# Kernel tuning notes

Hardware: AMD Instinct MI355X
Metric: run time of the kernel (lower is better)

The kernel has to match this reference:

```python
import jax, jax.numpy as jnp
import numpy as np

N_NODES = 100000
N_EDGES = 3200000
D_IN = 128
D_OUT = 128
EPS = 0.0  # GINConv default eps, not trained


def setup_inputs() -> dict:
    key = jax.random.key(0)
    k1, k2, k3, k4, k5, k6, k7 = jax.random.split(key, 7)
    x = jax.random.normal(k1, (N_NODES, D_IN), dtype=jnp.float32)
    edge_index = jax.random.randint(k2, (2, N_EDGES), 0, N_NODES, dtype=jnp.int64)
    # MLP params: Linear(D_IN->D_OUT), ReLU, Linear(D_OUT->D_OUT)
    s1 = 1.0 / np.sqrt(D_IN)
    s2 = 1.0 / np.sqrt(D_OUT)
    W1 = jax.random.uniform(k3, (D_IN, D_OUT), jnp.float32, -s1, s1)
    b1 = jax.random.uniform(k4, (D_OUT,), jnp.float32, -s1, s1)
    W2 = jax.random.uniform(k5, (D_OUT, D_OUT), jnp.float32, -s2, s2)
    b2 = jax.random.uniform(k6, (D_OUT,), jnp.float32, -s2, s2)
    return {"x": x, "edge_index": edge_index, "W1": W1, "b1": b1, "W2": W2, "b2": b2}


def reference(x, edge_index, W1, b1, W2, b2):
    src, dst = edge_index[0], edge_index[1]
    # message = x[src]; aggregate by sum onto dst (source_to_target flow)
    agg = jax.ops.segment_sum(x[src], dst, num_segments=x.shape[0])  # [N, D_IN]
    h = (1.0 + EPS) * x + agg
    h = jax.nn.relu(h @ W1 + b1)
    return h @ W2 + b2
```

## Files before the change

### kernel.cpp

```cpp
#include <hip/hip_runtime.h>

#define D 128
#define TILE_ROWS 64
#define MLP_THREADS 512
#define SCAN_THREADS 1024
#define BK_NODES 128
#define MAX_BKT 1024
#define EPB 16
#define SC_THREADS 512
#define SC_EPB 24
#define CAPL 6144
#define FMLP_THREADS 512
#define MLP_BM 128
#define HSTR 136

typedef unsigned short ushort_t;
typedef unsigned int uint_t;
typedef __attribute__((ext_vector_type(8))) short short8v;
typedef __attribute__((ext_vector_type(4))) float f32x4;

__device__ __forceinline__ ushort_t f2bf(float f) {
    uint_t u = __float_as_uint(f);
    u = u + 0x7FFFu + ((u >> 16) & 1u);
    return (ushort_t)(u >> 16);
}
__device__ __forceinline__ float bf_lo(uint_t u) { return __uint_as_float(u << 16); }
__device__ __forceinline__ float bf_hi(uint_t u) { return __uint_as_float(u & 0xffff0000u); }

__global__ void cast_kernel(const float* __restrict__ x, ushort_t* __restrict__ xh, int n4) {
    int i = blockIdx.x * blockDim.x + threadIdx.x;
    if (i < n4) {
        float4 v = reinterpret_cast<const float4*>(x)[i];
        ushort4 o;
        o.x = f2bf(v.x); o.y = f2bf(v.y); o.z = f2bf(v.z); o.w = f2bf(v.w);
        reinterpret_cast<ushort4*>(xh)[i] = o;
    }
}

__global__ void wprep_kernel(const float* __restrict__ W1, const float* __restrict__ W2,
                             ushort_t* __restrict__ w1t, ushort_t* __restrict__ w2t) {
    int i = blockIdx.x * blockDim.x + threadIdx.x;
    if (i < D * D) {
        int c = i & 127, k = i >> 7;
        w1t[(size_t)c * HSTR + k] = f2bf(W1[(size_t)k * D + c]);
        w2t[(size_t)c * HSTR + k] = f2bf(W2[(size_t)k * D + c]);
    }
}

__global__ void zero_kernel(int* __restrict__ p, int n) {
    int i = blockIdx.x * blockDim.x + threadIdx.x;
    if (i < n) p[i] = 0;
}

__global__ void coarse_hist_kernel(const int* __restrict__ dsts,
                                   int* __restrict__ ghist, int ne, int nbkt) {
    __shared__ int h[MAX_BKT];
    for (int k = threadIdx.x; k < nbkt; k += blockDim.x) h[k] = 0;
    __syncthreads();
    int base = blockIdx.x * blockDim.x * EPB;
    for (int j = 0; j < EPB; ++j) {
        int e = base + j * blockDim.x + threadIdx.x;
        if (e < ne) atomicAdd(&h[dsts[e] >> 7], 1);
    }
    __syncthreads();
    for (int k = threadIdx.x; k < nbkt; k += blockDim.x)
        if (h[k]) atomicAdd(&ghist[k], h[k]);
}

__global__ __launch_bounds__(SCAN_THREADS) void coarse_scan_kernel(
    const int* __restrict__ ghist, int* __restrict__ cbase,
    int* __restrict__ ccursor, int* __restrict__ offsets,
    int nbkt, int nnodes, int ne) {
    __shared__ int sc[SCAN_THREADS];
    int t = threadIdx.x;
    int v = (t < nbkt) ? ghist[t] : 0;
    sc[t] = v;
    __syncthreads();
    for (int off = 1; off < SCAN_THREADS; off <<= 1) {
        int u = (t >= off) ? sc[t - off] : 0;
        __syncthreads();
        sc[t] += u;
        __syncthreads();
    }
    if (t < nbkt) { cbase[t] = sc[t] - v; ccursor[t] = sc[t] - v; }
    if (t == 0) { cbase[nbkt] = sc[SCAN_THREADS - 1]; offsets[nnodes] = ne; }
}

__global__ __launch_bounds__(SC_THREADS) void coarse_scatter_kernel(
    const int* __restrict__ ei, int* __restrict__ ccursor,
    int* __restrict__ pairs, int ne, int nbkt) {
    __shared__ int h[MAX_BKT];
    __shared__ int lbase[MAX_BKT];
    __shared__ int gbase[MAX_BKT];
    __shared__ int lcur[MAX_BKT];
    __shared__ int stot[SC_THREADS];
    __shared__ int stage[SC_THREADS * SC_EPB];

    const int t = threadIdx.x;
    const int base = blockIdx.x * SC_THREADS * SC_EPB;

    for (int k = t; k < MAX_BKT; k += SC_THREADS) h[k] = 0;
    __syncthreads();

    for (int j = 0; j < SC_EPB; ++j) {
        int e = base + j * SC_THREADS + t;
        if (e < ne) atomicAdd(&h[ei[ne + e] >> 7], 1);
    }
    __syncthreads();

    int a0 = h[2 * t], a1 = h[2 * t + 1];
    stot[t] = a0 + a1;
    __syncthreads();
    for (int off = 1; off < SC_THREADS; off <<= 1) {
        int u = (t >= off) ? stot[t - off] : 0;
        __syncthreads();
        stot[t] += u;
        __syncthreads();
    }
    int bexc = stot[t] - (a0 + a1);
    lbase[2 * t] = bexc;
    lbase[2 * t + 1] = bexc + a0;
    lcur[2 * t] = bexc;
    lcur[2 * t + 1] = bexc + a0;
    __syncthreads();

    for (int k = t; k < MAX_BKT; k += SC_THREADS)
        gbase[k] = h[k] ? atomicAdd(&ccursor[k], h[k]) : 0;
    __syncthreads();

    for (int j = 0; j < SC_EPB; ++j) {
        int e = base + j * SC_THREADS + t;
        if (e < ne) {
            int dst = ei[ne + e];
            int src = ei[e];
            int k = dst >> 7;
            int pos = atomicAdd(&lcur[k], 1);
            stage[pos] = (src << 7) | (dst & (BK_NODES - 1));
        }
    }
    __syncthreads();

    const int lane = t & 63, w = t >> 6;
    for (int k = w; k < nbkt; k += (SC_THREADS / 64)) {
        int cnt = h[k];
        int lb = lbase[k], gb = gbase[k];
        for (int i = lane; i < cnt; i += 64)
            pairs[gb + i] = stage[lb + i];
    }
}

__global__ void bucket_csr_kernel(const int* __restrict__ pairs,
                                  const int* __restrict__ cbase,
                                  int* __restrict__ offsets,
                                  int* __restrict__ sorted_src,
                                  int nnodes) {
    __shared__ int h[BK_NODES];
    __shared__ int ex[BK_NODES];
    __shared__ int cur[BK_NODES];
    __shared__ int stage[CAPL];
    int b = blockIdx.x;
    int t = threadIdx.x;
    int rbeg = cbase[b], rend = cbase[b + 1];
    int cnt = rend - rbeg;
    if (t < BK_NODES) h[t] = 0;
    __syncthreads();
    for (int i = rbeg + t; i < rend; i += blockDim.x)
        atomicAdd(&h[pairs[i] & (BK_NODES - 1)], 1);
    __syncthreads();
    if (t < BK_NODES) ex[t] = h[t];
    __syncthreads();
    for (int off = 1; off < BK_NODES; off <<= 1) {
        int u = (t >= off && t < BK_NODES) ? ex[t - off] : 0;
        __syncthreads();
        if (t < BK_NODES) ex[t] += u;
        __syncthreads();
    }
    const bool staged = (cnt <= CAPL);
    if (t < BK_NODES) {
        int e = ex[t] - h[t];
        cur[t] = staged ? e : rbeg + e;
        int node = b * BK_NODES + t;
        if (node < nnodes) offsets[node] = rbeg + e;
    }
    __syncthreads();
    if (staged) {
        for (int i = rbeg + t; i < rend; i += blockDim.x) {
            int p = pairs[i];
            int pos = atomicAdd(&cur[p & (BK_NODES - 1)], 1);
            stage[pos] = p >> 7;
        }
        __syncthreads();
        for (int i = t; i < cnt; i += blockDim.x)
            sorted_src[rbeg + i] = stage[i];
    } else {
        for (int i = rbeg + t; i < rend; i += blockDim.x) {
            int p = pairs[i];
            int pos = atomicAdd(&cur[p & (BK_NODES - 1)], 1);
            sorted_src[pos] = p >> 7;
        }
    }
}

__global__ void agg_bf_kernel(const ushort_t* __restrict__ xh,
                              const int* __restrict__ sorted_src,
                              const int* __restrict__ offsets,
                              float* __restrict__ out,
                              uint_t* __restrict__ hbf, int nnodes) {
    int gid = blockIdx.x * blockDim.x + threadIdx.x;
    int node = gid >> 6;
    if (node >= nnodes) return;
    const int lane = threadIdx.x & 63;
    const int col = lane & 31;
    const int half = lane >> 5;
    const uint2* xp = reinterpret_cast<const uint2*>(xh);
    int beg = offsets[node];
    int end = offsets[node + 1];

    float s0, s1, s2, s3;
    {
        uint2 u = xp[(size_t)node * 32 + col];
        if (half) { u.x = 0u; u.y = 0u; }
        s0 = bf_lo(u.x); s1 = bf_hi(u.x);
        s2 = bf_lo(u.y); s3 = bf_hi(u.y);
    }

    int i = beg;
    for (; i + 16 <= end; i += 16) {
        uint2 v0 = xp[(size_t)sorted_src[i + 0 + half] * 32 + col];
        uint2 v1 = xp[(size_t)sorted_src[i + 2 + half] * 32 + col];
        uint2 v2 = xp[(size_t)sorted_src[i + 4 + half] * 32 + col];
        uint2 v3 = xp[(size_t)sorted_src[i + 6 + half] * 32 + col];
        uint2 v4 = xp[(size_t)sorted_src[i + 8 + half] * 32 + col];
        uint2 v5 = xp[(size_t)sorted_src[i + 10 + half] * 32 + col];
        uint2 v6 = xp[(size_t)sorted_src[i + 12 + half] * 32 + col];
        uint2 v7 = xp[(size_t)sorted_src[i + 14 + half] * 32 + col];
        s0 += bf_lo(v0.x) + bf_lo(v1.x) + bf_lo(v2.x) + bf_lo(v3.x) +
              bf_lo(v4.x) + bf_lo(v5.x) + bf_lo(v6.x) + bf_lo(v7.x);
        s1 += bf_hi(v0.x) + bf_hi(v1.x) + bf_hi(v2.x) + bf_hi(v3.x) +
              bf_hi(v4.x) + bf_hi(v5.x) + bf_hi(v6.x) + bf_hi(v7.x);
        s2 += bf_lo(v0.y) + bf_lo(v1.y) + bf_lo(v2.y) + bf_lo(v3.y) +
              bf_lo(v4.y) + bf_lo(v5.y) + bf_lo(v6.y) + bf_lo(v7.y);
        s3 += bf_hi(v0.y) + bf_hi(v1.y) + bf_hi(v2.y) + bf_hi(v3.y) +
              bf_hi(v4.y) + bf_hi(v5.y) + bf_hi(v6.y) + bf_hi(v7.y);
    }
    for (; i + 2 <= end; i += 2) {
        uint2 u = xp[(size_t)sorted_src[i + half] * 32 + col];
        s0 += bf_lo(u.x); s1 += bf_hi(u.x);
        s2 += bf_lo(u.y); s3 += bf_hi(u.y);
    }
    if (i < end && half == 0) {
        uint2 u = xp[(size_t)sorted_src[i] * 32 + col];
        s0 += bf_lo(u.x); s1 += bf_hi(u.x);
        s2 += bf_lo(u.y); s3 += bf_hi(u.y);
    }

    s0 += __shfl_xor(s0, 32);
    s1 += __shfl_xor(s1, 32);
    s2 += __shfl_xor(s2, 32);
    s3 += __shfl_xor(s3, 32);

    if (half == 0) {
        if (hbf) {
            uint_t lo = (uint_t)f2bf(s0) | ((uint_t)f2bf(s1) << 16);
            uint_t hi = (uint_t)f2bf(s2) | ((uint_t)f2bf(s3) << 16);
            uint2 o; o.x = lo; o.y = hi;
            reinterpret_cast<uint2*>(hbf)[(size_t)node * 32 + col] = o;
        } else {
            float4 o; o.x = s0; o.y = s1; o.z = s2; o.w = s3;
            reinterpret_cast<float4*>(out + (size_t)node * D)[col] = o;
        }
    }
}

__global__ void agg_fp_kernel(const float* __restrict__ x,
                              const int* __restrict__ sorted_src,
                              const int* __restrict__ offsets,
                              float* __restrict__ out, int nnodes) {
    int gid = blockIdx.x * blockDim.x + threadIdx.x;
    int node = gid >> 6;
    if (node >= nnodes) return;
    int lane = threadIdx.x & 63;
    int beg = offsets[node];
    int end = offsets[node + 1];
    const float2* xp = reinterpret_cast<const float2*>(x);
    float2 a = xp[(size_t)node * 64 + lane];
    float sx = a.x, sy = a.y;
    int i = beg;
    for (; i + 8 <= end; i += 8) {
        int s0 = sorted_src[i + 0], s1 = sorted_src[i + 1];
        int s2 = sorted_src[i + 2], s3 = sorted_src[i + 3];
        int s4 = sorted_src[i + 4], s5 = sorted_src[i + 5];
        int s6 = sorted_src[i + 6], s7 = sorted_src[i + 7];
        float2 v0 = xp[(size_t)s0 * 64 + lane];
        float2 v1 = xp[(size_t)s1 * 64 + lane];
        float2 v2 = xp[(size_t)s2 * 64 + lane];
        float2 v3 = xp[(size_t)s3 * 64 + lane];
        float2 v4 = xp[(size_t)s4 * 64 + lane];
        float2 v5 = xp[(size_t)s5 * 64 + lane];
        float2 v6 = xp[(size_t)s6 * 64 + lane];
        float2 v7 = xp[(size_t)s7 * 64 + lane];
        sx += ((v0.x + v1.x) + (v2.x + v3.x)) + ((v4.x + v5.x) + (v6.x + v7.x));
        sy += ((v0.y + v1.y) + (v2.y + v3.y)) + ((v4.y + v5.y) + (v6.y + v7.y));
    }
    for (; i < end; ++i) {
        float2 v = xp[(size_t)sorted_src[i] * 64 + lane];
        sx += v.x;
        sy += v.y;
    }
    float2 o; o.x = sx; o.y = sy;
    reinterpret_cast<float2*>(out)[(size_t)node * 64 + lane] = o;
}

template <bool BF>
__global__ __launch_bounds__(FMLP_THREADS, 1) void fused_mlp_kernel(
    const float* __restrict__ h, const uint_t* __restrict__ hbf,
    const ushort_t* __restrict__ w1t, const ushort_t* __restrict__ w2t,
    const float* __restrict__ b1, const float* __restrict__ b2,
    float* __restrict__ outp, int nrows) {
    __shared__ ushort_t sh[MLP_BM * HSTR];
    __shared__ ushort_t sw1[D * HSTR];
    __shared__ ushort_t sw2[D * HSTR];
    const int tid = threadIdx.x;
    const int row0 = blockIdx.x * MLP_BM;

    {
        const uint4* s1 = reinterpret_cast<const uint4*>(w1t);
        const uint4* s2 = reinterpret_cast<const uint4*>(w2t);
        uint4* d1 = reinterpret_cast<uint4*>(sw1);
        uint4* d2 = reinterpret_cast<uint4*>(sw2);
        for (int i = tid; i < D * HSTR / 8; i += FMLP_THREADS) { d1[i] = s1[i]; d2[i] = s2[i]; }
    }
    if (BF) {
        for (int i = tid; i < MLP_BM * 16; i += FMLP_THREADS) {
            int r = i >> 4, c = i & 15;
            uint4 v = make_uint4(0u, 0u, 0u, 0u);
            if (row0 + r < nrows)
                v = reinterpret_cast<const uint4*>(hbf + (size_t)(row0 + r) * 64)[c];
            *reinterpret_cast<uint4*>(&sh[r * HSTR + c * 8]) = v;
        }
    } else {
        for (int i = tid; i < MLP_BM * 32; i += FMLP_THREADS) {
            int r = i >> 5, c4 = i & 31;
            float4 v = make_float4(0.f, 0.f, 0.f, 0.f);
            if (row0 + r < nrows)
                v = reinterpret_cast<const float4*>(h + (size_t)(row0 + r) * D)[c4];
            ushort4 o;
            o.x = f2bf(v.x); o.y = f2bf(v.y); o.z = f2bf(v.z); o.w = f2bf(v.w);
            *reinterpret_cast<ushort4*>(&sh[r * HSTR + c4 * 4]) = o;
        }
    }
    __syncthreads();

    const int w = tid >> 6, l = tid & 63;
    const int lr = l & 15, lg = l >> 4;
    const int rowb = w * 16;

    short8v A[4];
#pragma unroll
    for (int kk = 0; kk < 4; ++kk)
        A[kk] = *reinterpret_cast<const short8v*>(&sh[(rowb + lr) * HSTR + kk * 32 + lg * 8]);
#pragma unroll
    for (int n = 0; n < 8; ++n) {
        float bv = b1[n * 16 + lr];
        f32x4 acc = {bv, bv, bv, bv};
#pragma unroll
        for (int kk = 0; kk < 4; ++kk) {
            short8v B = *reinterpret_cast<const short8v*>(&sw1[(n * 16 + lr) * HSTR + kk * 32 + lg * 8]);
            acc = __builtin_amdgcn_mfma_f32_16x16x32_bf16(A[kk], B, acc, 0, 0, 0);
        }
#pragma unroll
        for (int r = 0; r < 4; ++r) {
            float v = fmaxf(acc[r], 0.f);
            sh[(rowb + lg * 4 + r) * HSTR + n * 16 + lr] = f2bf(v);
        }
    }

    short8v A2[4];
#pragma unroll
    for (int kk = 0; kk < 4; ++kk)
        A2[kk] = *reinterpret_cast<const short8v*>(&sh[(rowb + lr) * HSTR + kk * 32 + lg * 8]);
#pragma unroll
    for (int n = 0; n < 8; ++n) {
        float bv = b2[n * 16 + lr];
        f32x4 acc = {bv, bv, bv, bv};
#pragma unroll
        for (int kk = 0; kk < 4; ++kk) {
            short8v B = *reinterpret_cast<const short8v*>(&sw2[(n * 16 + lr) * HSTR + kk * 32 + lg * 8]);
            acc = __builtin_amdgcn_mfma_f32_16x16x32_bf16(A2[kk], B, acc, 0, 0, 0);
        }
#pragma unroll
        for (int r = 0; r < 4; ++r) {
            int grow = row0 + rowb + lg * 4 + r;
            if (grow < nrows)
                outp[(size_t)grow * D + n * 16 + lr] = acc[r];
        }
    }
}

__global__ void init_kernel(const float* __restrict__ x, float* __restrict__ out, int n4) {
    int i = blockIdx.x * blockDim.x + threadIdx.x;
    if (i < n4) {
        reinterpret_cast<float4*>(out)[i] = reinterpret_cast<const float4*>(x)[i];
    }
}

__global__ void scatter_kernel(const float* __restrict__ x,
                               const int* __restrict__ ei,
                               float* __restrict__ out, int ne) {
    long long gid = (long long)blockIdx.x * blockDim.x + threadIdx.x;
    int e = (int)(gid >> 5);
    if (e >= ne) return;
    int d0 = ((int)gid & 31) * 4;
    int src = ei[e];
    int dst = ei[ne + e];
    float4 v = *reinterpret_cast<const float4*>(x + (long long)src * D + d0);
    float* o = out + (long long)dst * D + d0;
    atomicAdd(o + 0, v.x);
    atomicAdd(o + 1, v.y);
    atomicAdd(o + 2, v.z);
    atomicAdd(o + 3, v.w);
}

template <bool RELU>
__global__ __launch_bounds__(MLP_THREADS, 1) void mlp_kernel(
    const float* __restrict__ in, const float* __restrict__ W,
    const float* __restrict__ b, float* __restrict__ outp, int nrows) {
    __shared__ float Wl[D][D];
    __shared__ float inl[TILE_ROWS][D + 4];

    const int tid = threadIdx.x;
    const int row0 = blockIdx.x * TILE_ROWS;

    for (int i = tid; i < D * D / 4; i += MLP_THREADS) {
        reinterpret_cast<float4*>(&Wl[0][0])[i] =
            reinterpret_cast<const float4*>(W)[i];
    }
    for (int i = tid; i < TILE_ROWS * (D / 4); i += MLP_THREADS) {
        int r = i >> 5;
        int k4 = i & 31;
        float4 v = make_float4(0.f, 0.f, 0.f, 0.f);
        if (row0 + r < nrows)
            v = *reinterpret_cast<const float4*>(in + (size_t)(row0 + r) * D + 4 * k4);
        *reinterpret_cast<float4*>(&inl[r][4 * k4]) = v;
    }
    __syncthreads();

    const int cg = tid & 31;
    const int rg = tid >> 5;
    const int c0 = cg * 4;
    const int r0 = rg * 4;

    float4 bv = *reinterpret_cast<const float4*>(b + c0);
    float acc[4][4];
#pragma unroll
    for (int i = 0; i < 4; ++i) {
        acc[i][0] = bv.x; acc[i][1] = bv.y; acc[i][2] = bv.z; acc[i][3] = bv.w;
    }

#pragma unroll 4
    for (int k4 = 0; k4 < 32; ++k4) {
        float4 w0 = *reinterpret_cast<const float4*>(&Wl[4 * k4 + 0][c0]);
        float4 w1 = *reinterpret_cast<const float4*>(&Wl[4 * k4 + 1][c0]);
        float4 w2 = *reinterpret_cast<const float4*>(&Wl[4 * k4 + 2][c0]);
        float4 w3 = *reinterpret_cast<const float4*>(&Wl[4 * k4 + 3][c0]);
#pragma unroll
        for (int i = 0; i < 4; ++i) {
            float4 a = *reinterpret_cast<const float4*>(&inl[r0 + i][4 * k4]);
            acc[i][0] += a.x * w0.x + a.y * w1.x + a.z * w2.x + a.w * w3.x;
            acc[i][1] += a.x * w0.y + a.y * w1.y + a.z * w2.y + a.w * w3.y;
            acc[i][2] += a.x * w0.z + a.y * w1.z + a.z * w2.z + a.w * w3.z;
            acc[i][3] += a.x * w0.w + a.y * w1.w + a.z * w2.w + a.w * w3.w;
        }
    }

#pragma unroll
    for (int i = 0; i < 4; ++i) {
        int r = row0 + r0 + i;
        if (r < nrows) {
            float4 o;
            if (RELU) {
                o.x = fmaxf(acc[i][0], 0.f); o.y = fmaxf(acc[i][1], 0.f);
                o.z = fmaxf(acc[i][2], 0.f); o.w = fmaxf(acc[i][3], 0.f);
            } else {
                o.x = acc[i][0]; o.y = acc[i][1]; o.z = acc[i][2]; o.w = acc[i][3];
            }
            *reinterpret_cast<float4*>(outp + (size_t)r * D + c0) = o;
        }
    }
}

extern "C" void kernel_launch(void* const* d_in, const int* in_sizes, int n_in,
                              void* d_out, int out_size, void* d_ws, size_t ws_size,
                              hipStream_t stream) {
    const float* x = (const float*)d_in[0];
    const int* ei = (const int*)d_in[1];
    const float* W1 = (const float*)d_in[2];
    const float* b1 = (const float*)d_in[3];
    const float* W2 = (const float*)d_in[4];
    const float* b2 = (const float*)d_in[5];
    float* out = (float*)d_out;

    const int nrows = in_sizes[0] / D;
    const int ne = in_sizes[1] / 2;
    const int nbkt = (nrows + BK_NODES - 1) / BK_NODES;

    size_t xh_bytes = (((size_t)nrows * D * sizeof(ushort_t)) + 15) & ~(size_t)15;
    size_t csr_bytes = ((size_t)(nrows + 1) + 2 * (size_t)ne + 3 * (size_t)nbkt + 1) * sizeof(int);
    size_t need_fp = csr_bytes;
    size_t need_bf = xh_bytes + csr_bytes;
    size_t wt_bytes = (size_t)D * HSTR * sizeof(ushort_t);
    size_t wt_off = (need_bf + 15) & ~(size_t)15;
    size_t need_mfma = wt_off + 2 * wt_bytes;
    size_t hbf_off = (need_mfma + 15) & ~(size_t)15;
    size_t hbf_bytes = (size_t)nrows * D * sizeof(ushort_t);
    size_t need_hbf = hbf_off + hbf_bytes;

    const int hblocks = (ne + 256 * EPB - 1) / (256 * EPB);
    const int sblocks2 = (ne + SC_THREADS * SC_EPB - 1) / (SC_THREADS * SC_EPB);

    bool use_mfma = false;
    bool use_hbf = false;
    ushort_t* w1t = nullptr;
    ushort_t* w2t = nullptr;
    uint_t* hbf = nullptr;

    if (nbkt <= MAX_BKT && ws_size >= need_fp) {
        const bool bf = (ws_size >= need_bf);
        use_mfma = (ws_size >= need_mfma);
        use_hbf = bf && use_mfma && (ws_size >= need_hbf);
        char* wp = (char*)d_ws;
        ushort_t* xh = nullptr;
        if (bf) { xh = (ushort_t*)wp; wp += xh_bytes; }
        int* offsets = (int*)wp;
        int* sorted_src = offsets + (nrows + 1);
        int* pairs = sorted_src + ne;
        int* ghist = pairs + ne;
        int* cbase = ghist + nbkt;
        int* ccursor = cbase + (nbkt + 1);
        if (use_mfma) {
            w1t = (ushort_t*)((char*)d_ws + wt_off);
            w2t = (ushort_t*)((char*)d_ws + wt_off + wt_bytes);
        }
        if (use_hbf) hbf = (uint_t*)((char*)d_ws + hbf_off);

        if (bf) {
            int n4 = nrows * (D / 4);
            cast_kernel<<<(n4 + 255) / 256, 256, 0, stream>>>(x, xh, n4);
        }
        if (use_mfma)
            wprep_kernel<<<(D * D + 255) / 256, 256, 0, stream>>>(W1, W2, w1t, w2t);
        zero_kernel<<<(nbkt + 255) / 256, 256, 0, stream>>>(ghist, nbkt);
        coarse_hist_kernel<<<hblocks, 256, 0, stream>>>(ei + ne, ghist, ne, nbkt);
        coarse_scan_kernel<<<1, SCAN_THREADS, 0, stream>>>(ghist, cbase, ccursor,
                                                           offsets, nbkt, nrows, ne);
        coarse_scatter_kernel<<<sblocks2, SC_THREADS, 0, stream>>>(ei, ccursor, pairs, ne, nbkt);
        bucket_csr_kernel<<<nbkt, 256, 0, stream>>>(pairs, cbase, offsets, sorted_src, nrows);

        long long athreads = (long long)nrows * 64;
        int ablocks = (int)((athreads + 255) / 256);
        if (bf)
            agg_bf_kernel<<<ablocks, 256, 0, stream>>>(xh, sorted_src, offsets, out, hbf, nrows);
        else
            agg_fp_kernel<<<ablocks, 256, 0, stream>>>(x, sorted_src, offsets, out, nrows);
    } else {
        int n4 = nrows * (D / 4);
        init_kernel<<<(n4 + 255) / 256, 256, 0, stream>>>(x, out, n4);
        long long sthreads = (long long)ne * 32;
        scatter_kernel<<<(int)((sthreads + 255) / 256), 256, 0, stream>>>(x, ei, out, ne);
    }

    if (use_mfma) {
        int fblocks = (nrows + MLP_BM - 1) / MLP_BM;
        if (use_hbf)
            fused_mlp_kernel<true><<<fblocks, FMLP_THREADS, 0, stream>>>(
                out, hbf, w1t, w2t, b1, b2, out, nrows);
        else
            fused_mlp_kernel<false><<<fblocks, FMLP_THREADS, 0, stream>>>(
                out, nullptr, w1t, w2t, b1, b2, out, nrows);
    } else {
        int mblocks = (nrows + TILE_ROWS - 1) / TILE_ROWS;
        mlp_kernel<true><<<mblocks, MLP_THREADS, 0, stream>>>(out, W1, b1, out, nrows);
        mlp_kernel<false><<<mblocks, MLP_THREADS, 0, stream>>>(out, W2, b2, out, nrows);
    }
}
```

Measured before the change: 244.6 us.

## Fuse cast, histogram and weight prep into one prologue; fold scan into scatter

Merges the bf16 cast, coarse destination histogram and weight transpose into a single block-partitioned prologue kernel, and replaces the zero kernel with a memset of ghist and the cursors. The separate single-block scan kernel is removed; every scatter block redundantly scans the global histogram and adds the bucket base to a cursor that now starts at zero. Bucket CSR is launched with 512 threads instead of 256. The aim is to cut kernel launches and the serial single-block scan, at the cost of a redundant scan in each scatter block.

```diff
diff --git a/kernel.cpp b/kernel.cpp
--- a/kernel.cpp
+++ b/kernel.cpp
@@ -3,12 +3,14 @@
 #define D 128
 #define TILE_ROWS 64
 #define MLP_THREADS 512
-#define SCAN_THREADS 1024
 #define BK_NODES 128
 #define MAX_BKT 1024
 #define EPB 16
+#define PRO_THREADS 256
+#define CAST_VEC 4
 #define SC_THREADS 512
 #define SC_EPB 24
+#define BC_THREADS 512
 #define CAPL 6144
 #define FMLP_THREADS 512
 #define MLP_BM 128
@@ -27,69 +29,57 @@
 __device__ __forceinline__ float bf_lo(uint_t u) { return __uint_as_float(u << 16); }
 __device__ __forceinline__ float bf_hi(uint_t u) { return __uint_as_float(u & 0xffff0000u); }
 
-__global__ void cast_kernel(const float* __restrict__ x, ushort_t* __restrict__ xh, int n4) {
-    int i = blockIdx.x * blockDim.x + threadIdx.x;
-    if (i < n4) {
-        float4 v = reinterpret_cast<const float4*>(x)[i];
-        ushort4 o;
-        o.x = f2bf(v.x); o.y = f2bf(v.y); o.z = f2bf(v.z); o.w = f2bf(v.w);
-        reinterpret_cast<ushort4*>(xh)[i] = o;
-    }
-}
-
-__global__ void wprep_kernel(const float* __restrict__ W1, const float* __restrict__ W2,
-                             ushort_t* __restrict__ w1t, ushort_t* __restrict__ w2t) {
-    int i = blockIdx.x * blockDim.x + threadIdx.x;
-    if (i < D * D) {
+__global__ __launch_bounds__(PRO_THREADS) void prologue_kernel(
+    const float* __restrict__ x, ushort_t* __restrict__ xh, int n4, int cast_blocks,
+    const int* __restrict__ dsts, int* __restrict__ ghist, int ne, int nbkt, int hist_blocks,
+    const float* __restrict__ W1, const float* __restrict__ W2,
+    ushort_t* __restrict__ w1t, ushort_t* __restrict__ w2t) {
+    __shared__ int h[MAX_BKT];
+    int b = blockIdx.x;
+    if (b < cast_blocks) {
+        int base = b * PRO_THREADS * CAST_VEC + threadIdx.x;
+#pragma unroll
+        for (int j = 0; j < CAST_VEC; ++j) {
+            int i = base + j * PRO_THREADS;
+            if (i < n4) {
+                float4 v = reinterpret_cast<const float4*>(x)[i];
+                ushort4 o;
+                o.x = f2bf(v.x); o.y = f2bf(v.y); o.z = f2bf(v.z); o.w = f2bf(v.w);
+                reinterpret_cast<ushort4*>(xh)[i] = o;
+            }
+        }
+        return;
+    }
+    b -= cast_blocks;
+    if (b < hist_blocks) {
+        for (int k = threadIdx.x; k < nbkt; k += PRO_THREADS) h[k] = 0;
+        __syncthreads();
+        int base = b * PRO_THREADS * EPB;
+        for (int j = 0; j < EPB; ++j) {
+            int e = base + j * PRO_THREADS + threadIdx.x;
+            if (e < ne) atomicAdd(&h[dsts[e] >> 7], 1);
+        }
+        __syncthreads();
+        for (int k = threadIdx.x; k < nbkt; k += PRO_THREADS)
+            if (h[k]) atomicAdd(&ghist[k], h[k]);
+        return;
+    }
+    b -= hist_blocks;
+    int i = b * PRO_THREADS + threadIdx.x;
+    if (w1t != nullptr && i < D * D) {
         int c = i & 127, k = i >> 7;
         w1t[(size_t)c * HSTR + k] = f2bf(W1[(size_t)k * D + c]);
         w2t[(size_t)c * HSTR + k] = f2bf(W2[(size_t)k * D + c]);
     }
 }
 
-__global__ void zero_kernel(int* __restrict__ p, int n) {
-    int i = blockIdx.x * blockDim.x + threadIdx.x;
-    if (i < n) p[i] = 0;
-}
-
-__global__ void coarse_hist_kernel(const int* __restrict__ dsts,
-                                   int* __restrict__ ghist, int ne, int nbkt) {
+__global__ __launch_bounds__(SC_THREADS) void coarse_scatter_kernel(
+    const int* __restrict__ ei, const int* __restrict__ ghist,
+    int* __restrict__ cbase, int* __restrict__ ccursor,
+    int* __restrict__ offsets, int* __restrict__ pairs,
+    int ne, int nbkt, int nnodes) {
     __shared__ int h[MAX_BKT];
-    for (int k = threadIdx.x; k < nbkt; k += blockDim.x) h[k] = 0;
-    __syncthreads();
-    int base = blockIdx.x * blockDim.x * EPB;
-    for (int j = 0; j < EPB; ++j) {
-        int e = base + j * blockDim.x + threadIdx.x;
-        if (e < ne) atomicAdd(&h[dsts[e] >> 7], 1);
-    }
-    __syncthreads();
-    for (int k = threadIdx.x; k < nbkt; k += blockDim.x)
-        if (h[k]) atomicAdd(&ghist[k], h[k]);
-}
-
-__global__ __launch_bounds__(SCAN_THREADS) void coarse_scan_kernel(
-    const int* __restrict__ ghist, int* __restrict__ cbase,
-    int* __restrict__ ccursor, int* __restrict__ offsets,
-    int nbkt, int nnodes, int ne) {
-    __shared__ int sc[SCAN_THREADS];
-    int t = threadIdx.x;
-    int v = (t < nbkt) ? ghist[t] : 0;
-    sc[t] = v;
-    __syncthreads();
-    for (int off = 1; off < SCAN_THREADS; off <<= 1) {
-        int u = (t >= off) ? sc[t - off] : 0;
-        __syncthreads();
-        sc[t] += u;
-        __syncthreads();
-    }
-    if (t < nbkt) { cbase[t] = sc[t] - v; ccursor[t] = sc[t] - v; }
-    if (t == 0) { cbase[nbkt] = sc[SCAN_THREADS - 1]; offsets[nnodes] = ne; }
-}
-
-__global__ __launch_bounds__(SC_THREADS) void coarse_scatter_kernel(
-    const int* __restrict__ ei, int* __restrict__ ccursor,
-    int* __restrict__ pairs, int ne, int nbkt) {
-    __shared__ int h[MAX_BKT];
+    __shared__ int cbl[MAX_BKT];
     __shared__ int lbase[MAX_BKT];
     __shared__ int gbase[MAX_BKT];
     __shared__ int lcur[MAX_BKT];
@@ -99,9 +89,30 @@
     const int t = threadIdx.x;
     const int base = blockIdx.x * SC_THREADS * SC_EPB;
 
+    int g0 = (2 * t < nbkt) ? ghist[2 * t] : 0;
+    int g1 = (2 * t + 1 < nbkt) ? ghist[2 * t + 1] : 0;
+    stot[t] = g0 + g1;
+    __syncthreads();
+    for (int off = 1; off < SC_THREADS; off <<= 1) {
+        int u = (t >= off) ? stot[t - off] : 0;
+        __syncthreads();
+        stot[t] += u;
+        __syncthreads();
+    }
+    {
+        int ge = stot[t] - (g0 + g1);
+        cbl[2 * t] = ge;
+        cbl[2 * t + 1] = ge + g0;
+        if (blockIdx.x == 0) {
+            if (2 * t < nbkt) cbase[2 * t] = ge;
+            if (2 * t + 1 < nbkt) cbase[2 * t + 1] = ge + g0;
+            if (t == SC_THREADS - 1) { cbase[nbkt] = stot[t]; offsets[nnodes] = ne; }
+        }
+    }
+    __syncthreads();
+
     for (int k = t; k < MAX_BKT; k += SC_THREADS) h[k] = 0;
     __syncthreads();
-
     for (int j = 0; j < SC_EPB; ++j) {
         int e = base + j * SC_THREADS + t;
         if (e < ne) atomicAdd(&h[ei[ne + e] >> 7], 1);
@@ -118,14 +129,12 @@
         __syncthreads();
     }
     int bexc = stot[t] - (a0 + a1);
-    lbase[2 * t] = bexc;
-    lbase[2 * t + 1] = bexc + a0;
-    lcur[2 * t] = bexc;
-    lcur[2 * t + 1] = bexc + a0;
+    lbase[2 * t] = bexc;          lcur[2 * t] = bexc;
+    lbase[2 * t + 1] = bexc + a0; lcur[2 * t + 1] = bexc + a0;
     __syncthreads();
 
     for (int k = t; k < MAX_BKT; k += SC_THREADS)
-        gbase[k] = h[k] ? atomicAdd(&ccursor[k], h[k]) : 0;
+        gbase[k] = h[k] ? (cbl[k] + atomicAdd(&ccursor[k], h[k])) : 0;
     __syncthreads();
 
     for (int j = 0; j < SC_EPB; ++j) {
@@ -149,11 +158,9 @@
     }
 }
 
-__global__ void bucket_csr_kernel(const int* __restrict__ pairs,
-                                  const int* __restrict__ cbase,
-                                  int* __restrict__ offsets,
-                                  int* __restrict__ sorted_src,
-                                  int nnodes) {
+__global__ __launch_bounds__(BC_THREADS) void bucket_csr_kernel(
+    const int* __restrict__ pairs, const int* __restrict__ cbase,
+    int* __restrict__ offsets, int* __restrict__ sorted_src, int nnodes) {
     __shared__ int h[BK_NODES];
     __shared__ int ex[BK_NODES];
     __shared__ int cur[BK_NODES];
@@ -515,8 +522,9 @@
     size_t hbf_bytes = (size_t)nrows * D * sizeof(ushort_t);
     size_t need_hbf = hbf_off + hbf_bytes;
 
-    const int hblocks = (ne + 256 * EPB - 1) / (256 * EPB);
-    const int sblocks2 = (ne + SC_THREADS * SC_EPB - 1) / (SC_THREADS * SC_EPB);
+    const int n4 = nrows * (D / 4);
+    const int hist_blocks = (ne + PRO_THREADS * EPB - 1) / (PRO_THREADS * EPB);
+    const int sc_blocks = (ne + SC_THREADS * SC_EPB - 1) / (SC_THREADS * SC_EPB);
 
     bool use_mfma = false;
     bool use_hbf = false;
@@ -543,18 +551,18 @@
         }
         if (use_hbf) hbf = (uint_t*)((char*)d_ws + hbf_off);
 
-        if (bf) {
-            int n4 = nrows * (D / 4);
-            cast_kernel<<<(n4 + 255) / 256, 256, 0, stream>>>(x, xh, n4);
-        }
-        if (use_mfma)
-            wprep_kernel<<<(D * D + 255) / 256, 256, 0, stream>>>(W1, W2, w1t, w2t);
-        zero_kernel<<<(nbkt + 255) / 256, 256, 0, stream>>>(ghist, nbkt);
-        coarse_hist_kernel<<<hblocks, 256, 0, stream>>>(ei + ne, ghist, ne, nbkt);
-        coarse_scan_kernel<<<1, SCAN_THREADS, 0, stream>>>(ghist, cbase, ccursor,
-                                                           offsets, nbkt, nrows, ne);
-        coarse_scatter_kernel<<<sblocks2, SC_THREADS, 0, stream>>>(ei, ccursor, pairs, ne, nbkt);
-        bucket_csr_kernel<<<nbkt, 256, 0, stream>>>(pairs, cbase, offsets, sorted_src, nrows);
+        hipMemsetAsync(ghist, 0, (size_t)(3 * nbkt + 1) * sizeof(int), stream);
+
+        const int cast_blocks = bf ? (n4 + PRO_THREADS * CAST_VEC - 1) / (PRO_THREADS * CAST_VEC) : 0;
+        const int wprep_blocks = use_mfma ? (D * D + PRO_THREADS - 1) / PRO_THREADS : 0;
+        const int pro_blocks = cast_blocks + hist_blocks + wprep_blocks;
+        prologue_kernel<<<pro_blocks, PRO_THREADS, 0, stream>>>(
+            x, xh, n4, cast_blocks, ei + ne, ghist, ne, nbkt, hist_blocks,
+            W1, W2, w1t, w2t);
+
+        coarse_scatter_kernel<<<sc_blocks, SC_THREADS, 0, stream>>>(
+            ei, ghist, cbase, ccursor, offsets, pairs, ne, nbkt, nrows);
+        bucket_csr_kernel<<<nbkt, BC_THREADS, 0, stream>>>(pairs, cbase, offsets, sorted_src, nrows);
 
         long long athreads = (long long)nrows * 64;
         int ablocks = (int)((athreads + 255) / 256);
@@ -563,7 +571,6 @@
         else
             agg_fp_kernel<<<ablocks, 256, 0, stream>>>(x, sorted_src, offsets, out, nrows);
     } else {
-        int n4 = nrows * (D / 4);
         init_kernel<<<(n4 + 255) / 256, 256, 0, stream>>>(x, out, n4);
         long long sthreads = (long long)ne * 32;
         scatter_kernel<<<(int)((sthreads + 255) / 256), 256, 0, stream>>>(x, ei, out, ne);
```

New measurement: 241.4 us. No clear change (-1.3%).
